# Optimization experiments

Hardware: AMD Instinct MI355X
Metric: run time of the kernel (lower is better)

The kernel has to match this reference:

```python
import jax, jax.numpy as jnp
import numpy as np

EPS_ATTN = 1e-6
EPS_LN = 1e-5


def _layer_norm(x, g, b):
    m = jnp.mean(x, axis=-1, keepdims=True)
    v = jnp.mean((x - m) ** 2, axis=-1, keepdims=True)
    return (x - m) * jax.lax.rsqrt(v + EPS_LN) * g + b


def _linear_attention(q, k, v):
    # q,k,v: [N, L/S, H, D]; elu feature map (+1 keeps values positive)
    q = jax.nn.elu(q) + 1.0
    k = jax.nn.elu(k) + 1.0
    s_len = v.shape[1]
    v = v / s_len
    kv = jnp.einsum('nshd,nshv->nhdv', k, v)            # [N,H,D,D]
    z = 1.0 / (jnp.einsum('nlhd,nhd->nlh', q, k.sum(axis=1)) + EPS_ATTN)
    out = jnp.einsum('nlhd,nhdv->nlhv', q, kv) * z[..., None] * s_len
    return out


def setup_inputs() -> dict:
    key = jax.random.key(0)
    ks = jax.random.split(key, 8)
    N, L, S, H, D = 4, 4096, 4096, 8, 64
    sc = 0.05
    return {
        'x': jax.random.normal(ks[0], (N, L, H, D), jnp.float32),
        'source': jax.random.normal(ks[1], (N, S, H, D), jnp.float32),
        'wq': jax.random.normal(ks[2], (D, D), jnp.float32) * sc,
        'wk': jax.random.normal(ks[3], (D, D), jnp.float32) * sc,
        'wv': jax.random.normal(ks[4], (D, D), jnp.float32) * sc,
        'wmerge': jax.random.normal(ks[5], (D, D), jnp.float32) * sc,
        'w1': jax.random.normal(ks[6], (2 * D, 2 * D), jnp.float32) * sc,
        'w2': jax.random.normal(ks[7], (D, 2 * D), jnp.float32) * sc,
        'g1': jnp.ones((D,), jnp.float32),
        'b1': jnp.zeros((D,), jnp.float32),
        'g2': jnp.ones((D,), jnp.float32),
        'b2': jnp.zeros((D,), jnp.float32),
    }


def reference(x, source, wq, wk, wv, wmerge, w1, w2, g1, b1, g2, b2):
    # projections (torch Linear: y = x @ W.T), applied on last dim D=d_model
    q = jnp.einsum('nlhd,ed->nlhe', x, wq)
    k = jnp.einsum('nshd,ed->nshe', source, wk)
    v = jnp.einsum('nshd,ed->nshe', source, wv)
    message = _linear_attention(q, k, v)                # [N,L,H,D]
    message = jnp.einsum('nlhd,ed->nlhe', message, wmerge)
    message = _layer_norm(message, g1, b1)
    h = jnp.concatenate([x, message], axis=-1)          # [N,L,H,2D]
    h = jax.nn.relu(jnp.einsum('nlhd,ed->nlhe', h, w1))
    h = jnp.einsum('nlhd,ed->nlhe', h, w2)              # [N,L,H,D]
    h = _layer_norm(h, g2, b2)
    return x + h
```

## Files before the change

### kernel.cpp

```cpp
#include <hip/hip_runtime.h>
#include <cstdint>

#define NB 4
#define LL 4096
#define SS 4096
#define HH 8
#define DD 64
#define NHC (NB*HH)

typedef unsigned short ushort_t;
typedef __bf16 bf16x8 __attribute__((ext_vector_type(8)));
typedef float f32x4 __attribute__((ext_vector_type(4)));
typedef unsigned short u16x8 __attribute__((ext_vector_type(8)));

__device__ __forceinline__ float bf2f(unsigned short u) {
    union { unsigned int i; float f; } v; v.i = ((unsigned int)u) << 16; return v.f;
}
__device__ __forceinline__ unsigned short f2bf(float f) {
    union { float ff; unsigned int i; } v; v.ff = f;
    unsigned int x = v.i;
    x += 0x7fffu + ((x >> 16) & 1u);
    return (unsigned short)(x >> 16);
}
__device__ __forceinline__ bool input_is_bf16(const void* g1) {
    return ((const unsigned short*)g1)[0] == 0x3F80u;
}

template<bool BF16>
__device__ __forceinline__ float ldgf(const void* p, size_t i) {
    if constexpr (BF16) return bf2f(((const unsigned short*)p)[i]);
    else                return ((const float*)p)[i];
}
template<bool BF16>
__device__ __forceinline__ u16x8 ld8(const void* p, size_t i) {
    if constexpr (BF16) {
        return *reinterpret_cast<const u16x8*>((const unsigned short*)p + i);
    } else {
        const float* f = (const float*)p + i;
        u16x8 o;
        #pragma unroll
        for (int j = 0; j < 8; ++j) o[j] = f2bf(f[j]);
        return o;
    }
}
__device__ __forceinline__ bf16x8 ldsA(const ushort_t* p) {
    return *reinterpret_cast<const bf16x8*>(p);
}
#define MFMA16(a,b,c) __builtin_amdgcn_mfma_f32_16x16x32_bf16(a,b,c,0,0,0)

template<bool BF16, int LC>
__device__ __forceinline__ void stage_w(const void* g, size_t goff, ushort_t* dst,
                                        int rows, int dstride, int tid) {
    int total8 = (rows << LC) >> 3;
    for (int i8 = tid; i8 < total8; i8 += 256) {
        int i = i8 << 3;
        int r = i >> LC, c = i & ((1 << LC) - 1);
        *reinterpret_cast<u16x8*>(dst + r * dstride + c) = ld8<BF16>(g, goff + i);
    }
}

__device__ __forceinline__ void red16(float v[4]) {
    #pragma unroll
    for (int m = 1; m < 16; m <<= 1) {
        #pragma unroll
        for (int r = 0; r < 4; ++r) v[r] += __shfl_xor(v[r], m);
    }
}

template<bool BF16>
__global__ __launch_bounds__(256, 2) void kv_kernel(
    const void* __restrict__ src, const void* __restrict__ wk, const void* __restrict__ wv,
    const void* __restrict__ g1, float* __restrict__ kvg, float* __restrict__ ksumg)
{
    if (input_is_bf16(g1) != BF16) return;
    __shared__ ushort_t S[128 * 72];
    __shared__ ushort_t KT[64 * 136];
    __shared__ ushort_t VT[64 * 136];

    const int tid = threadIdx.x;
    const int lane = tid & 63, w = tid >> 6;
    const int lg = lane >> 4, l15 = lane & 15;
    const int bid = blockIdx.x;
    const int nh = bid >> 3, ch = bid & 7;
    const int n = nh >> 3, h = nh & 7;
    const int s0 = ch * 512;
    const f32x4 z4 = {0.f, 0.f, 0.f, 0.f};

    stage_w<BF16, 6>(wk, 0, KT, 64, 136, tid);
    stage_w<BF16, 6>(wv, 0, VT, 64, 136, tid);
    __syncthreads();
    bf16x8 wkf[2][4], wvf[2][4];
    #pragma unroll
    for (int ks = 0; ks < 2; ++ks)
        #pragma unroll
        for (int nt = 0; nt < 4; ++nt) {
            wkf[ks][nt] = ldsA(KT + (nt * 16 + l15) * 136 + ks * 32 + lg * 8);
            wvf[ks][nt] = ldsA(VT + (nt * 16 + l15) * 136 + ks * 32 + lg * 8);
        }
    __syncthreads();

    float ksp[4] = {0.f, 0.f, 0.f, 0.f};
    f32x4 kvacc[4];
    #pragma unroll
    for (int nt = 0; nt < 4; ++nt) kvacc[nt] = z4;

    for (int st = 0; st < 4; ++st) {
        for (int i = tid; i < 128 * 8; i += 256) {
            int r = i >> 3, c8 = (i & 7) << 3;
            size_t gb = ((size_t)((size_t)n * SS + (s0 + st * 128 + r)) * HH + h) * DD + c8;
            *reinterpret_cast<u16x8*>(S + r * 72 + c8) = ld8<BF16>(src, gb);
        }
        __syncthreads();

        #pragma unroll
        for (int mtt = 0; mtt < 2; ++mtt) {
            const int rowA = w * 32 + mtt * 16;
            bf16x8 af[2];
            #pragma unroll
            for (int ks = 0; ks < 2; ++ks)
                af[ks] = ldsA(S + (rowA + l15) * 72 + ks * 32 + lg * 8);
            f32x4 ka[4], va[4];
            #pragma unroll
            for (int nt = 0; nt < 4; ++nt) { ka[nt] = z4; va[nt] = z4; }
            #pragma unroll
            for (int ks = 0; ks < 2; ++ks)
                #pragma unroll
                for (int nt = 0; nt < 4; ++nt) {
                    ka[nt] = MFMA16(af[ks], wkf[ks][nt], ka[nt]);
                    va[nt] = MFMA16(af[ks], wvf[ks][nt], va[nt]);
                }
            #pragma unroll
            for (int nt = 0; nt < 4; ++nt)
                #pragma unroll
                for (int r = 0; r < 4; ++r) {
                    float kvl = ka[nt][r];
                    kvl = kvl > 0.f ? kvl + 1.f : __expf(kvl);
                    ksp[nt] += kvl;
                    int srow = rowA + lg * 4 + r;
                    int dcol = nt * 16 + l15;
                    KT[dcol * 136 + srow] = f2bf(kvl);
                    VT[dcol * 136 + srow] = f2bf(va[nt][r]);
                }
        }
        __syncthreads();

        #pragma unroll
        for (int ks = 0; ks < 4; ++ks) {
            bf16x8 akv = ldsA(KT + (w * 16 + l15) * 136 + ks * 32 + lg * 8);
            #pragma unroll
            for (int nt = 0; nt < 4; ++nt) {
                bf16x8 bkv = ldsA(VT + (nt * 16 + l15) * 136 + ks * 32 + lg * 8);
                kvacc[nt] = MFMA16(akv, bkv, kvacc[nt]);
            }
        }
        __syncthreads();
    }

    float* kvo = kvg + (size_t)nh * DD * DD;
    #pragma unroll
    for (int nt = 0; nt < 4; ++nt)
        #pragma unroll
        for (int r = 0; r < 4; ++r)
            atomicAdd(&kvo[(w * 16 + lg * 4 + r) * DD + nt * 16 + l15], kvacc[nt][r]);
    #pragma unroll
    for (int m = 16; m < 64; m <<= 1)
        #pragma unroll
        for (int nt = 0; nt < 4; ++nt) ksp[nt] += __shfl_xor(ksp[nt], m);
    if (lane < 16) {
        #pragma unroll
        for (int nt = 0; nt < 4; ++nt)
            atomicAdd(&ksumg[nh * DD + nt * 16 + lane], ksp[nt]);
    }
}

template<bool BF16>
__global__ __launch_bounds__(256, 2) void main_kernel(
    const void* __restrict__ x,
    const void* __restrict__ wq, const void* __restrict__ wm,
    const void* __restrict__ w1, const void* __restrict__ w2,
    const void* __restrict__ g1, const void* __restrict__ b1,
    const void* __restrict__ g2, const void* __restrict__ b2,
    const float* __restrict__ kvg, const float* __restrict__ ksumg,
    void* __restrict__ outp)
{
    if (input_is_bf16(g1) != BF16) return;
    __shared__ ushort_t w1s[128 * 136];
    __shared__ ushort_t kvs[64 * 72];
    __shared__ ushort_t B0[64 * 72];
    __shared__ ushort_t B1[64 * 72];
    __shared__ ushort_t B2[64 * 136];

    const int tid = threadIdx.x;
    const int lane = tid & 63, w = tid >> 6;
    const int lg = lane >> 4, l15 = lane & 15;
    const int bid = blockIdx.x;
    const int nh = bid >> 4, ch = bid & 15;
    const int n = nh >> 3, h = nh & 7;
    const int rowA = w * 16;
    const f32x4 z4 = {0.f, 0.f, 0.f, 0.f};

    for (int i = tid; i < 4096; i += 256) {
        int d = i >> 6, e = i & 63;
        kvs[e * 72 + d] = f2bf(kvg[(size_t)nh * 4096 + i]);
    }
    stage_w<BF16, 7>(w1, 0, w1s, 128, 136, tid);

    bf16x8 wqf[2][4], wmf[2][4], w2f[4][4];
    stage_w<BF16, 6>(wq, 0, B0, 64, 72, tid);
    __syncthreads();
    #pragma unroll
    for (int ks = 0; ks < 2; ++ks)
        #pragma unroll
        for (int nt = 0; nt < 4; ++nt)
            wqf[ks][nt] = ldsA(B0 + (nt * 16 + l15) * 72 + ks * 32 + lg * 8);
    __syncthreads();
    stage_w<BF16, 6>(wm, 0, B0, 64, 72, tid);
    __syncthreads();
    #pragma unroll
    for (int ks = 0; ks < 2; ++ks)
        #pragma unroll
        for (int nt = 0; nt < 4; ++nt)
            wmf[ks][nt] = ldsA(B0 + (nt * 16 + l15) * 72 + ks * 32 + lg * 8);
    __syncthreads();
    stage_w<BF16, 7>(w2, 0, B2, 64, 136, tid);
    __syncthreads();
    #pragma unroll
    for (int ks = 0; ks < 4; ++ks)
        #pragma unroll
        for (int nt = 0; nt < 4; ++nt)
            w2f[ks][nt] = ldsA(B2 + (nt * 16 + l15) * 136 + ks * 32 + lg * 8);

    float g1r[4], b1r[4], g2r[4], b2r[4], ksr[4];
    #pragma unroll
    for (int nt = 0; nt < 4; ++nt) {
        int c = nt * 16 + l15;
        g1r[nt] = ldgf<BF16>(g1, c); b1r[nt] = ldgf<BF16>(b1, c);
        g2r[nt] = ldgf<BF16>(g2, c); b2r[nt] = ldgf<BF16>(b2, c);
        ksr[nt] = ksumg[nh * 64 + c];
    }
    __syncthreads();

    for (int t = 0; t < 4; ++t) {
        const int l0 = ch * 256 + t * 64;

        #pragma unroll
        for (int p = 0; p < 2; ++p) {
            int r16 = p * 8 + (lane >> 3), c8 = (lane & 7) << 3;
            size_t gb = ((size_t)((size_t)n * LL + (l0 + rowA + r16)) * HH + h) * DD + c8;
            *reinterpret_cast<u16x8*>(B0 + (rowA + r16) * 72 + c8) = ld8<BF16>(x, gb);
        }

        bf16x8 af[2];
        #pragma unroll
        for (int ks = 0; ks < 2; ++ks)
            af[ks] = ldsA(B0 + (rowA + l15) * 72 + ks * 32 + lg * 8);
        f32x4 qa[4];
        #pragma unroll
        for (int nt = 0; nt < 4; ++nt) qa[nt] = z4;
        #pragma unroll
        for (int ks = 0; ks < 2; ++ks)
            #pragma unroll
            for (int nt = 0; nt < 4; ++nt)
                qa[nt] = MFMA16(af[ks], wqf[ks][nt], qa[nt]);
        float zp[4] = {0.f, 0.f, 0.f, 0.f};
        #pragma unroll
        for (int nt = 0; nt < 4; ++nt)
            #pragma unroll
            for (int r = 0; r < 4; ++r) {
                float v = qa[nt][r];
                v = v > 0.f ? v + 1.f : __expf(v);
                qa[nt][r] = v;
                zp[r] += v * ksr[nt];
            }
        red16(zp);
        float zr[4];
        #pragma unroll
        for (int r = 0; r < 4; ++r) zr[r] = 1.f / (zp[r] + 1e-6f);
        #pragma unroll
        for (int nt = 0; nt < 4; ++nt)
            #pragma unroll
            for (int r = 0; r < 4; ++r)
                B1[(rowA + lg * 4 + r) * 72 + nt * 16 + l15] = f2bf(qa[nt][r]);

        #pragma unroll
        for (int ks = 0; ks < 2; ++ks)
            af[ks] = ldsA(B1 + (rowA + l15) * 72 + ks * 32 + lg * 8);
        f32x4 ma[4];
        #pragma unroll
        for (int nt = 0; nt < 4; ++nt) ma[nt] = z4;
        #pragma unroll
        for (int ks = 0; ks < 2; ++ks)
            #pragma unroll
            for (int nt = 0; nt < 4; ++nt) {
                bf16x8 bkv = ldsA(kvs + (nt * 16 + l15) * 72 + ks * 32 + lg * 8);
                ma[nt] = MFMA16(af[ks], bkv, ma[nt]);
            }
        #pragma unroll
        for (int nt = 0; nt < 4; ++nt)
            #pragma unroll
            for (int r = 0; r < 4; ++r)
                B1[(rowA + lg * 4 + r) * 72 + nt * 16 + l15] = f2bf(ma[nt][r] * zr[r]);

        #pragma unroll
        for (int ks = 0; ks < 2; ++ks)
            af[ks] = ldsA(B1 + (rowA + l15) * 72 + ks * 32 + lg * 8);
        f32x4 ga[4];
        #pragma unroll
        for (int nt = 0; nt < 4; ++nt) ga[nt] = z4;
        #pragma unroll
        for (int ks = 0; ks < 2; ++ks)
            #pragma unroll
            for (int nt = 0; nt < 4; ++nt)
                ga[nt] = MFMA16(af[ks], wmf[ks][nt], ga[nt]);
        float s1[4] = {0.f,0.f,0.f,0.f}, s2[4] = {0.f,0.f,0.f,0.f};
        #pragma unroll
        for (int nt = 0; nt < 4; ++nt)
            #pragma unroll
            for (int r = 0; r < 4; ++r) {
                float v = ga[nt][r]; s1[r] += v; s2[r] += v * v;
            }
        red16(s1); red16(s2);
        #pragma unroll
        for (int r = 0; r < 4; ++r) {
            float mu = s1[r] * 0.015625f;
            float var = s2[r] * 0.015625f - mu * mu;
            float rs = rsqrtf(var + 1e-5f);
            s1[r] = mu; s2[r] = rs;
        }
        #pragma unroll
        for (int nt = 0; nt < 4; ++nt)
            #pragma unroll
            for (int r = 0; r < 4; ++r)
                B1[(rowA + lg * 4 + r) * 72 + nt * 16 + l15] =
                    f2bf((ga[nt][r] - s1[r]) * s2[r] * g1r[nt] + b1r[nt]);

        #pragma unroll
        for (int half = 0; half < 2; ++half) {
            f32x4 ta[4];
            #pragma unroll
            for (int nt = 0; nt < 4; ++nt) ta[nt] = z4;
            #pragma unroll
            for (int ks = 0; ks < 4; ++ks) {
                const ushort_t* basep = (ks < 2) ? B0 : B1;
                bf16x8 a1 = ldsA(basep + (rowA + l15) * 72 + (ks & 1) * 32 + lg * 8);
                #pragma unroll
                for (int nt = 0; nt < 4; ++nt) {
                    bf16x8 bw = ldsA(w1s + (half * 64 + nt * 16 + l15) * 136 + ks * 32 + lg * 8);
                    ta[nt] = MFMA16(a1, bw, ta[nt]);
                }
            }
            #pragma unroll
            for (int nt = 0; nt < 4; ++nt)
                #pragma unroll
                for (int r = 0; r < 4; ++r)
                    B2[(rowA + lg * 4 + r) * 136 + (half * 4 + nt) * 16 + l15] =
                        f2bf(fmaxf(ta[nt][r], 0.f));
        }

        f32x4 ha[4];
        #pragma unroll
        for (int nt = 0; nt < 4; ++nt) ha[nt] = z4;
        #pragma unroll
        for (int ks = 0; ks < 4; ++ks) {
            bf16x8 a2 = ldsA(B2 + (rowA + l15) * 136 + ks * 32 + lg * 8);
            #pragma unroll
            for (int nt = 0; nt < 4; ++nt)
                ha[nt] = MFMA16(a2, w2f[ks][nt], ha[nt]);
        }
        float t1[4] = {0.f,0.f,0.f,0.f}, t2[4] = {0.f,0.f,0.f,0.f};
        #pragma unroll
        for (int nt = 0; nt < 4; ++nt)
            #pragma unroll
            for (int r = 0; r < 4; ++r) {
                float v = ha[nt][r]; t1[r] += v; t2[r] += v * v;
            }
        red16(t1); red16(t2);
        #pragma unroll
        for (int r = 0; r < 4; ++r) {
            float mu = t1[r] * 0.015625f;
            float var = t2[r] * 0.015625f - mu * mu;
            float rs = rsqrtf(var + 1e-5f);
            t1[r] = mu; t2[r] = rs;
        }
        #pragma unroll
        for (int nt = 0; nt < 4; ++nt)
            #pragma unroll
            for (int r = 0; r < 4; ++r) {
                float xv = bf2f(B0[(rowA + lg * 4 + r) * 72 + nt * 16 + l15]);
                float ov = xv + (ha[nt][r] - t1[r]) * t2[r] * g2r[nt] + b2r[nt];
                B1[(rowA + lg * 4 + r) * 72 + nt * 16 + l15] = f2bf(ov);
            }

        #pragma unroll
        for (int p = 0; p < 2; ++p) {
            int r16 = p * 8 + (lane >> 3), c8 = (lane & 7) << 3;
            size_t gb = ((size_t)((size_t)n * LL + (l0 + rowA + r16)) * HH + h) * DD + c8;
            u16x8 v = *reinterpret_cast<const u16x8*>(B1 + (rowA + r16) * 72 + c8);
            if constexpr (BF16) {
                *reinterpret_cast<u16x8*>((unsigned short*)outp + gb) = v;
            } else {
                float* fo = (float*)outp + gb;
                #pragma unroll
                for (int j = 0; j < 8; ++j) fo[j] = bf2f(v[j]);
            }
        }
    }
}

extern "C" void kernel_launch(void* const* d_in, const int* in_sizes, int n_in,
                              void* d_out, int out_size, void* d_ws, size_t ws_size,
                              hipStream_t stream) {
    const void* x   = d_in[0];
    const void* src = d_in[1];
    const void* wq  = d_in[2];
    const void* wk  = d_in[3];
    const void* wv  = d_in[4];
    const void* wm  = d_in[5];
    const void* w1  = d_in[6];
    const void* w2  = d_in[7];
    const void* g1  = d_in[8];
    const void* b1  = d_in[9];
    const void* g2  = d_in[10];
    const void* b2  = d_in[11];

    float* kvg   = (float*)d_ws;
    float* ksumg = kvg + (size_t)NHC * DD * DD;

    hipMemsetAsync(d_ws, 0, ((size_t)NHC * DD * DD + NHC * DD) * sizeof(float), stream);

    kv_kernel<true ><<<NHC * 8, 256, 0, stream>>>(src, wk, wv, g1, kvg, ksumg);
    kv_kernel<false><<<NHC * 8, 256, 0, stream>>>(src, wk, wv, g1, kvg, ksumg);
    main_kernel<true ><<<NHC * 16, 256, 0, stream>>>(x, wq, wm, w1, w2, g1, b1, g2, b2,
                                                     kvg, ksumg, d_out);
    main_kernel<false><<<NHC * 16, 256, 0, stream>>>(x, wq, wm, w1, w2, g1, b1, g2, b2,
                                                     kvg, ksumg, d_out);
}
```

Before: 170.3 us.

## Fold merge weight into KV matrix, single dtype-dispatch launches, split FFN by halves

Precomputes kv·Wmerge^T once per block so the per-tile merge projection GEMM and one LDS round-trip disappear, and the folded matrix is held in registers as MFMA B fragments. The two template launches per stage are collapsed into one kernel each that branches on input dtype at runtime, removing two empty kernel launches. The FFN second GEMM is interleaved per half so B2 shrinks to 64x72, cutting LDS use. Folding changes rounding order (kv·Wm rounded to bf16) and moves the z scaling before the merge, which is mathematically equivalent.

```diff
diff --git a/kernel.cpp b/kernel.cpp
--- a/kernel.cpp
+++ b/kernel.cpp
@@ -68,15 +68,11 @@
 }
 
 template<bool BF16>
-__global__ __launch_bounds__(256, 2) void kv_kernel(
-    const void* __restrict__ src, const void* __restrict__ wk, const void* __restrict__ wv,
-    const void* __restrict__ g1, float* __restrict__ kvg, float* __restrict__ ksumg)
+__device__ void kv_body(const void* __restrict__ src, const void* __restrict__ wk,
+                        const void* __restrict__ wv, float* __restrict__ kvg,
+                        float* __restrict__ ksumg,
+                        ushort_t* S, ushort_t* KT, ushort_t* VT)
 {
-    if (input_is_bf16(g1) != BF16) return;
-    __shared__ ushort_t S[128 * 72];
-    __shared__ ushort_t KT[64 * 136];
-    __shared__ ushort_t VT[64 * 136];
-
     const int tid = threadIdx.x;
     const int lane = tid & 63, w = tid >> 6;
     const int lg = lane >> 4, l15 = lane & 15;
@@ -99,10 +95,10 @@
         }
     __syncthreads();
 
+    f32x4 kvacc[4];
+    #pragma unroll
+    for (int nt = 0; nt < 4; ++nt) kvacc[nt] = z4;
     float ksp[4] = {0.f, 0.f, 0.f, 0.f};
-    f32x4 kvacc[4];
-    #pragma unroll
-    for (int nt = 0; nt < 4; ++nt) kvacc[nt] = z4;
 
     for (int st = 0; st < 4; ++st) {
         for (int i = tid; i < 128 * 8; i += 256) {
@@ -173,7 +169,243 @@
     }
 }
 
+__global__ __launch_bounds__(256, 2) void kv_kernel(
+    const void* __restrict__ src, const void* __restrict__ wk, const void* __restrict__ wv,
+    const void* __restrict__ g1, float* __restrict__ kvg, float* __restrict__ ksumg)
+{
+    __shared__ ushort_t S[128 * 72];
+    __shared__ ushort_t KT[64 * 136];
+    __shared__ ushort_t VT[64 * 136];
+    if (input_is_bf16(g1)) kv_body<true >(src, wk, wv, kvg, ksumg, S, KT, VT);
+    else                   kv_body<false>(src, wk, wv, kvg, ksumg, S, KT, VT);
+}
+
 template<bool BF16>
+__device__ void main_body(const void* __restrict__ x,
+                          const void* __restrict__ wq, const void* __restrict__ wm,
+                          const void* __restrict__ w1, const void* __restrict__ w2,
+                          const void* __restrict__ g1, const void* __restrict__ b1,
+                          const void* __restrict__ g2, const void* __restrict__ b2,
+                          const float* __restrict__ kvg, const float* __restrict__ ksumg,
+                          void* __restrict__ outp,
+                          ushort_t* w1s, ushort_t* kvs, ushort_t* B0, ushort_t* B1,
+                          ushort_t* B2)
+{
+    const int tid = threadIdx.x;
+    const int lane = tid & 63, w = tid >> 6;
+    const int lg = lane >> 4, l15 = lane & 15;
+    const int bid = blockIdx.x;
+    const int nh = bid >> 4, ch = bid & 15;
+    const int n = nh >> 3, h = nh & 7;
+    const int rowA = w * 16;
+    const f32x4 z4 = {0.f, 0.f, 0.f, 0.f};
+
+    stage_w<BF16, 6>(wq, 0, B0, 64, 72, tid);
+    stage_w<BF16, 6>(wm, 0, B1, 64, 72, tid);
+    stage_w<BF16, 7>(w2, 0, w1s, 64, 136, tid);
+    for (int i = tid; i < 4096; i += 256) {
+        int d = i >> 6, e = i & 63;
+        B2[d * 72 + e] = f2bf(kvg[(size_t)nh * 4096 + i]);
+    }
+    __syncthreads();
+
+    bf16x8 wqf[2][4], w2f[4][4];
+    #pragma unroll
+    for (int ks = 0; ks < 2; ++ks)
+        #pragma unroll
+        for (int nt = 0; nt < 4; ++nt)
+            wqf[ks][nt] = ldsA(B0 + (nt * 16 + l15) * 72 + ks * 32 + lg * 8);
+    #pragma unroll
+    for (int ks = 0; ks < 4; ++ks)
+        #pragma unroll
+        for (int nt = 0; nt < 4; ++nt)
+            w2f[ks][nt] = ldsA(w1s + (nt * 16 + l15) * 136 + ks * 32 + lg * 8);
+    {
+        bf16x8 akv[2];
+        #pragma unroll
+        for (int ks = 0; ks < 2; ++ks)
+            akv[ks] = ldsA(B2 + (w * 16 + l15) * 72 + ks * 32 + lg * 8);
+        f32x4 km[4];
+        #pragma unroll
+        for (int nt = 0; nt < 4; ++nt) km[nt] = z4;
+        #pragma unroll
+        for (int ks = 0; ks < 2; ++ks)
+            #pragma unroll
+            for (int nt = 0; nt < 4; ++nt) {
+                bf16x8 bwm = ldsA(B1 + (nt * 16 + l15) * 72 + ks * 32 + lg * 8);
+                km[nt] = MFMA16(akv[ks], bwm, km[nt]);
+            }
+        #pragma unroll
+        for (int nt = 0; nt < 4; ++nt)
+            #pragma unroll
+            for (int r = 0; r < 4; ++r)
+                kvs[(nt * 16 + l15) * 72 + w * 16 + lg * 4 + r] = f2bf(km[nt][r]);
+    }
+    __syncthreads();
+
+    stage_w<BF16, 7>(w1, 0, w1s, 128, 136, tid);
+    bf16x8 kvmf[2][4];
+    #pragma unroll
+    for (int ks = 0; ks < 2; ++ks)
+        #pragma unroll
+        for (int nt = 0; nt < 4; ++nt)
+            kvmf[ks][nt] = ldsA(kvs + (nt * 16 + l15) * 72 + ks * 32 + lg * 8);
+    float g1r[4], b1r[4], g2r[4], b2r[4], ksr[4];
+    #pragma unroll
+    for (int nt = 0; nt < 4; ++nt) {
+        int c = nt * 16 + l15;
+        g1r[nt] = ldgf<BF16>(g1, c); b1r[nt] = ldgf<BF16>(b1, c);
+        g2r[nt] = ldgf<BF16>(g2, c); b2r[nt] = ldgf<BF16>(b2, c);
+        ksr[nt] = ksumg[nh * 64 + c];
+    }
+    __syncthreads();
+
+    for (int t = 0; t < 4; ++t) {
+        const int l0 = ch * 256 + t * 64;
+
+        #pragma unroll
+        for (int p = 0; p < 2; ++p) {
+            int r16 = p * 8 + (lane >> 3), c8 = (lane & 7) << 3;
+            size_t gb = ((size_t)((size_t)n * LL + (l0 + rowA + r16)) * HH + h) * DD + c8;
+            *reinterpret_cast<u16x8*>(B0 + (rowA + r16) * 72 + c8) = ld8<BF16>(x, gb);
+        }
+
+        bf16x8 af[2];
+        #pragma unroll
+        for (int ks = 0; ks < 2; ++ks)
+            af[ks] = ldsA(B0 + (rowA + l15) * 72 + ks * 32 + lg * 8);
+        f32x4 qa[4];
+        #pragma unroll
+        for (int nt = 0; nt < 4; ++nt) qa[nt] = z4;
+        #pragma unroll
+        for (int ks = 0; ks < 2; ++ks)
+            #pragma unroll
+            for (int nt = 0; nt < 4; ++nt)
+                qa[nt] = MFMA16(af[ks], wqf[ks][nt], qa[nt]);
+        float zp[4] = {0.f, 0.f, 0.f, 0.f};
+        #pragma unroll
+        for (int nt = 0; nt < 4; ++nt)
+            #pragma unroll
+            for (int r = 0; r < 4; ++r) {
+                float v = qa[nt][r];
+                v = v > 0.f ? v + 1.f : __expf(v);
+                zp[r] += v * ksr[nt];
+                B1[(rowA + lg * 4 + r) * 72 + nt * 16 + l15] = f2bf(v);
+            }
+        red16(zp);
+        float zr[4];
+        #pragma unroll
+        for (int r = 0; r < 4; ++r) zr[r] = 1.f / (zp[r] + 1e-6f);
+
+        #pragma unroll
+        for (int ks = 0; ks < 2; ++ks)
+            af[ks] = ldsA(B1 + (rowA + l15) * 72 + ks * 32 + lg * 8);
+        f32x4 ma[4];
+        #pragma unroll
+        for (int nt = 0; nt < 4; ++nt) ma[nt] = z4;
+        #pragma unroll
+        for (int ks = 0; ks < 2; ++ks)
+            #pragma unroll
+            for (int nt = 0; nt < 4; ++nt)
+                ma[nt] = MFMA16(af[ks], kvmf[ks][nt], ma[nt]);
+        #pragma unroll
+        for (int nt = 0; nt < 4; ++nt)
+            #pragma unroll
+            for (int r = 0; r < 4; ++r) ma[nt][r] *= zr[r];
+
+        float s1[4] = {0.f,0.f,0.f,0.f}, s2[4] = {0.f,0.f,0.f,0.f};
+        #pragma unroll
+        for (int nt = 0; nt < 4; ++nt)
+            #pragma unroll
+            for (int r = 0; r < 4; ++r) {
+                float v = ma[nt][r]; s1[r] += v; s2[r] += v * v;
+            }
+        red16(s1); red16(s2);
+        #pragma unroll
+        for (int r = 0; r < 4; ++r) {
+            float mu = s1[r] * 0.015625f;
+            float var = s2[r] * 0.015625f - mu * mu;
+            s1[r] = mu; s2[r] = rsqrtf(var + 1e-5f);
+        }
+        #pragma unroll
+        for (int nt = 0; nt < 4; ++nt)
+            #pragma unroll
+            for (int r = 0; r < 4; ++r)
+                B1[(rowA + lg * 4 + r) * 72 + nt * 16 + l15] =
+                    f2bf((ma[nt][r] - s1[r]) * s2[r] * g1r[nt] + b1r[nt]);
+
+        f32x4 ha[4];
+        #pragma unroll
+        for (int nt = 0; nt < 4; ++nt) ha[nt] = z4;
+        #pragma unroll
+        for (int half = 0; half < 2; ++half) {
+            f32x4 ta[4];
+            #pragma unroll
+            for (int nt = 0; nt < 4; ++nt) ta[nt] = z4;
+            #pragma unroll
+            for (int ks = 0; ks < 4; ++ks) {
+                const ushort_t* bp = (ks < 2) ? B0 : B1;
+                bf16x8 a1 = ldsA(bp + (rowA + l15) * 72 + (ks & 1) * 32 + lg * 8);
+                #pragma unroll
+                for (int nt = 0; nt < 4; ++nt) {
+                    bf16x8 bw = ldsA(w1s + (half * 64 + nt * 16 + l15) * 136 + ks * 32 + lg * 8);
+                    ta[nt] = MFMA16(a1, bw, ta[nt]);
+                }
+            }
+            #pragma unroll
+            for (int nt = 0; nt < 4; ++nt)
+                #pragma unroll
+                for (int r = 0; r < 4; ++r)
+                    B2[(rowA + lg * 4 + r) * 72 + nt * 16 + l15] =
+                        f2bf(fmaxf(ta[nt][r], 0.f));
+            #pragma unroll
+            for (int k2 = 0; k2 < 2; ++k2) {
+                bf16x8 a2 = ldsA(B2 + (rowA + l15) * 72 + k2 * 32 + lg * 8);
+                #pragma unroll
+                for (int nt = 0; nt < 4; ++nt)
+                    ha[nt] = MFMA16(a2, w2f[half * 2 + k2][nt], ha[nt]);
+            }
+        }
+
+        float t1[4] = {0.f,0.f,0.f,0.f}, t2[4] = {0.f,0.f,0.f,0.f};
+        #pragma unroll
+        for (int nt = 0; nt < 4; ++nt)
+            #pragma unroll
+            for (int r = 0; r < 4; ++r) {
+                float v = ha[nt][r]; t1[r] += v; t2[r] += v * v;
+            }
+        red16(t1); red16(t2);
+        #pragma unroll
+        for (int r = 0; r < 4; ++r) {
+            float mu = t1[r] * 0.015625f;
+            float var = t2[r] * 0.015625f - mu * mu;
+            t1[r] = mu; t2[r] = rsqrtf(var + 1e-5f);
+        }
+        #pragma unroll
+        for (int nt = 0; nt < 4; ++nt)
+            #pragma unroll
+            for (int r = 0; r < 4; ++r) {
+                float xv = bf2f(B0[(rowA + lg * 4 + r) * 72 + nt * 16 + l15]);
+                float ov = xv + (ha[nt][r] - t1[r]) * t2[r] * g2r[nt] + b2r[nt];
+                B1[(rowA + lg * 4 + r) * 72 + nt * 16 + l15] = f2bf(ov);
+            }
+
+        #pragma unroll
+        for (int p = 0; p < 2; ++p) {
+            int r16 = p * 8 + (lane >> 3), c8 = (lane & 7) << 3;
+            size_t gb = ((size_t)((size_t)n * LL + (l0 + rowA + r16)) * HH + h) * DD + c8;
+            u16x8 v = *reinterpret_cast<const u16x8*>(B1 + (rowA + r16) * 72 + c8);
+            if constexpr (BF16) {
+                *reinterpret_cast<u16x8*>((unsigned short*)outp + gb) = v;
+            } else {
+                float* fo = (float*)outp + gb;
+                #pragma unroll
+                for (int j = 0; j < 8; ++j) fo[j] = bf2f(v[j]);
+            }
+        }
+    }
+}
+
 __global__ __launch_bounds__(256, 2) void main_kernel(
     const void* __restrict__ x,
     const void* __restrict__ wq, const void* __restrict__ wm,
@@ -183,228 +415,17 @@
     const float* __restrict__ kvg, const float* __restrict__ ksumg,
     void* __restrict__ outp)
 {
-    if (input_is_bf16(g1) != BF16) return;
     __shared__ ushort_t w1s[128 * 136];
     __shared__ ushort_t kvs[64 * 72];
     __shared__ ushort_t B0[64 * 72];
     __shared__ ushort_t B1[64 * 72];
-    __shared__ ushort_t B2[64 * 136];
-
-    const int tid = threadIdx.x;
-    const int lane = tid & 63, w = tid >> 6;
-    const int lg = lane >> 4, l15 = lane & 15;
-    const int bid = blockIdx.x;
-    const int nh = bid >> 4, ch = bid & 15;
-    const int n = nh >> 3, h = nh & 7;
-    const int rowA = w * 16;
-    const f32x4 z4 = {0.f, 0.f, 0.f, 0.f};
-
-    for (int i = tid; i < 4096; i += 256) {
-        int d = i >> 6, e = i & 63;
-        kvs[e * 72 + d] = f2bf(kvg[(size_t)nh * 4096 + i]);
-    }
-    stage_w<BF16, 7>(w1, 0, w1s, 128, 136, tid);
-
-    bf16x8 wqf[2][4], wmf[2][4], w2f[4][4];
-    stage_w<BF16, 6>(wq, 0, B0, 64, 72, tid);
-    __syncthreads();
-    #pragma unroll
-    for (int ks = 0; ks < 2; ++ks)
-        #pragma unroll
-        for (int nt = 0; nt < 4; ++nt)
-            wqf[ks][nt] = ldsA(B0 + (nt * 16 + l15) * 72 + ks * 32 + lg * 8);
-    __syncthreads();
-    stage_w<BF16, 6>(wm, 0, B0, 64, 72, tid);
-    __syncthreads();
-    #pragma unroll
-    for (int ks = 0; ks < 2; ++ks)
-        #pragma unroll
-        for (int nt = 0; nt < 4; ++nt)
-            wmf[ks][nt] = ldsA(B0 + (nt * 16 + l15) * 72 + ks * 32 + lg * 8);
-    __syncthreads();
-    stage_w<BF16, 7>(w2, 0, B2, 64, 136, tid);
-    __syncthreads();
-    #pragma unroll
-    for (int ks = 0; ks < 4; ++ks)
-        #pragma unroll
-        for (int nt = 0; nt < 4; ++nt)
-            w2f[ks][nt] = ldsA(B2 + (nt * 16 + l15) * 136 + ks * 32 + lg * 8);
-
-    float g1r[4], b1r[4], g2r[4], b2r[4], ksr[4];
-    #pragma unroll
-    for (int nt = 0; nt < 4; ++nt) {
-        int c = nt * 16 + l15;
-        g1r[nt] = ldgf<BF16>(g1, c); b1r[nt] = ldgf<BF16>(b1, c);
-        g2r[nt] = ldgf<BF16>(g2, c); b2r[nt] = ldgf<BF16>(b2, c);
-        ksr[nt] = ksumg[nh * 64 + c];
-    }
-    __syncthreads();
-
-    for (int t = 0; t < 4; ++t) {
-        const int l0 = ch * 256 + t * 64;
-
-        #pragma unroll
-        for (int p = 0; p < 2; ++p) {
-            int r16 = p * 8 + (lane >> 3), c8 = (lane & 7) << 3;
-            size_t gb = ((size_t)((size_t)n * LL + (l0 + rowA + r16)) * HH + h) * DD + c8;
-            *reinterpret_cast<u16x8*>(B0 + (rowA + r16) * 72 + c8) = ld8<BF16>(x, gb);
-        }
-
-        bf16x8 af[2];
-        #pragma unroll
-        for (int ks = 0; ks < 2; ++ks)
-            af[ks] = ldsA(B0 + (rowA + l15) * 72 + ks * 32 + lg * 8);
-        f32x4 qa[4];
-        #pragma unroll
-        for (int nt = 0; nt < 4; ++nt) qa[nt] = z4;
-        #pragma unroll
-        for (int ks = 0; ks < 2; ++ks)
-            #pragma unroll
-            for (int nt = 0; nt < 4; ++nt)
-                qa[nt] = MFMA16(af[ks], wqf[ks][nt], qa[nt]);
-        float zp[4] = {0.f, 0.f, 0.f, 0.f};
-        #pragma unroll
-        for (int nt = 0; nt < 4; ++nt)
-            #pragma unroll
-            for (int r = 0; r < 4; ++r) {
-                float v = qa[nt][r];
-                v = v > 0.f ? v + 1.f : __expf(v);
-                qa[nt][r] = v;
-                zp[r] += v * ksr[nt];
-            }
-        red16(zp);
-        float zr[4];
-        #pragma unroll
-        for (int r = 0; r < 4; ++r) zr[r] = 1.f / (zp[r] + 1e-6f);
-        #pragma unroll
-        for (int nt = 0; nt < 4; ++nt)
-            #pragma unroll
-            for (int r = 0; r < 4; ++r)
-                B1[(rowA + lg * 4 + r) * 72 + nt * 16 + l15] = f2bf(qa[nt][r]);
-
-        #pragma unroll
-        for (int ks = 0; ks < 2; ++ks)
-            af[ks] = ldsA(B1 + (rowA + l15) * 72 + ks * 32 + lg * 8);
-        f32x4 ma[4];
-        #pragma unroll
-        for (int nt = 0; nt < 4; ++nt) ma[nt] = z4;
-        #pragma unroll
-        for (int ks = 0; ks < 2; ++ks)
-            #pragma unroll
-            for (int nt = 0; nt < 4; ++nt) {
-                bf16x8 bkv = ldsA(kvs + (nt * 16 + l15) * 72 + ks * 32 + lg * 8);
-                ma[nt] = MFMA16(af[ks], bkv, ma[nt]);
-            }
-        #pragma unroll
-        for (int nt = 0; nt < 4; ++nt)
-            #pragma unroll
-            for (int r = 0; r < 4; ++r)
-                B1[(rowA + lg * 4 + r) * 72 + nt * 16 + l15] = f2bf(ma[nt][r] * zr[r]);
-
-        #pragma unroll
-        for (int ks = 0; ks < 2; ++ks)
-            af[ks] = ldsA(B1 + (rowA + l15) * 72 + ks * 32 + lg * 8);
-        f32x4 ga[4];
-        #pragma unroll
-        for (int nt = 0; nt < 4; ++nt) ga[nt] = z4;
-        #pragma unroll
-        for (int ks = 0; ks < 2; ++ks)
-            #pragma unroll
-            for (int nt = 0; nt < 4; ++nt)
-                ga[nt] = MFMA16(af[ks], wmf[ks][nt], ga[nt]);
-        float s1[4] = {0.f,0.f,0.f,0.f}, s2[4] = {0.f,0.f,0.f,0.f};
-        #pragma unroll
-        for (int nt = 0; nt < 4; ++nt)
-            #pragma unroll
-            for (int r = 0; r < 4; ++r) {
-                float v = ga[nt][r]; s1[r] += v; s2[r] += v * v;
-            }
-        red16(s1); red16(s2);
-        #pragma unroll
-        for (int r = 0; r < 4; ++r) {
-            float mu = s1[r] * 0.015625f;
-            float var = s2[r] * 0.015625f - mu * mu;
-            float rs = rsqrtf(var + 1e-5f);
-            s1[r] = mu; s2[r] = rs;
-        }
-        #pragma unroll
-        for (int nt = 0; nt < 4; ++nt)
-            #pragma unroll
-            for (int r = 0; r < 4; ++r)
-                B1[(rowA + lg * 4 + r) * 72 + nt * 16 + l15] =
-                    f2bf((ga[nt][r] - s1[r]) * s2[r] * g1r[nt] + b1r[nt]);
-
-        #pragma unroll
-        for (int half = 0; half < 2; ++half) {
-            f32x4 ta[4];
-            #pragma unroll
-            for (int nt = 0; nt < 4; ++nt) ta[nt] = z4;
-            #pragma unroll
-            for (int ks = 0; ks < 4; ++ks) {
-                const ushort_t* basep = (ks < 2) ? B0 : B1;
-                bf16x8 a1 = ldsA(basep + (rowA + l15) * 72 + (ks & 1) * 32 + lg * 8);
-                #pragma unroll
-                for (int nt = 0; nt < 4; ++nt) {
-                    bf16x8 bw = ldsA(w1s + (half * 64 + nt * 16 + l15) * 136 + ks * 32 + lg * 8);
-                    ta[nt] = MFMA16(a1, bw, ta[nt]);
-                }
-            }
-            #pragma unroll
-            for (int nt = 0; nt < 4; ++nt)
-                #pragma unroll
-                for (int r = 0; r < 4; ++r)
-                    B2[(rowA + lg * 4 + r) * 136 + (half * 4 + nt) * 16 + l15] =
-                        f2bf(fmaxf(ta[nt][r], 0.f));
-        }
-
-        f32x4 ha[4];
-        #pragma unroll
-        for (int nt = 0; nt < 4; ++nt) ha[nt] = z4;
-        #pragma unroll
-        for (int ks = 0; ks < 4; ++ks) {
-            bf16x8 a2 = ldsA(B2 + (rowA + l15) * 136 + ks * 32 + lg * 8);
-            #pragma unroll
-            for (int nt = 0; nt < 4; ++nt)
-                ha[nt] = MFMA16(a2, w2f[ks][nt], ha[nt]);
-        }
-        float t1[4] = {0.f,0.f,0.f,0.f}, t2[4] = {0.f,0.f,0.f,0.f};
-        #pragma unroll
-        for (int nt = 0; nt < 4; ++nt)
-            #pragma unroll
-            for (int r = 0; r < 4; ++r) {
-                float v = ha[nt][r]; t1[r] += v; t2[r] += v * v;
-            }
-        red16(t1); red16(t2);
-        #pragma unroll
-        for (int r = 0; r < 4; ++r) {
-            float mu = t1[r] * 0.015625f;
-            float var = t2[r] * 0.015625f - mu * mu;
-            float rs = rsqrtf(var + 1e-5f);
-            t1[r] = mu; t2[r] = rs;
-        }
-        #pragma unroll
-        for (int nt = 0; nt < 4; ++nt)
-            #pragma unroll
-            for (int r = 0; r < 4; ++r) {
-                float xv = bf2f(B0[(rowA + lg * 4 + r) * 72 + nt * 16 + l15]);
-                float ov = xv + (ha[nt][r] - t1[r]) * t2[r] * g2r[nt] + b2r[nt];
-                B1[(rowA + lg * 4 + r) * 72 + nt * 16 + l15] = f2bf(ov);
-            }
-
-        #pragma unroll
-        for (int p = 0; p < 2; ++p) {
-            int r16 = p * 8 + (lane >> 3), c8 = (lane & 7) << 3;
-            size_t gb = ((size_t)((size_t)n * LL + (l0 + rowA + r16)) * HH + h) * DD + c8;
-            u16x8 v = *reinterpret_cast<const u16x8*>(B1 + (rowA + r16) * 72 + c8);
-            if constexpr (BF16) {
-                *reinterpret_cast<u16x8*>((unsigned short*)outp + gb) = v;
-            } else {
-                float* fo = (float*)outp + gb;
-                #pragma unroll
-                for (int j = 0; j < 8; ++j) fo[j] = bf2f(v[j]);
-            }
-        }
-    }
+    __shared__ ushort_t B2[64 * 72];
+    if (input_is_bf16(g1))
+        main_body<true >(x, wq, wm, w1, w2, g1, b1, g2, b2, kvg, ksumg, outp,
+                         w1s, kvs, B0, B1, B2);
+    else
+        main_body<false>(x, wq, wm, w1, w2, g1, b1, g2, b2, kvg, ksumg, outp,
+                         w1s, kvs, B0, B1, B2);
 }
 
 extern "C" void kernel_launch(void* const* d_in, const int* in_sizes, int n_in,
@@ -427,11 +448,7 @@
     float* ksumg = kvg + (size_t)NHC * DD * DD;
 
     hipMemsetAsync(d_ws, 0, ((size_t)NHC * DD * DD + NHC * DD) * sizeof(float), stream);
-
-    kv_kernel<true ><<<NHC * 8, 256, 0, stream>>>(src, wk, wv, g1, kvg, ksumg);
-    kv_kernel<false><<<NHC * 8, 256, 0, stream>>>(src, wk, wv, g1, kvg, ksumg);
-    main_kernel<true ><<<NHC * 16, 256, 0, stream>>>(x, wq, wm, w1, w2, g1, b1, g2, b2,
-                                                     kvg, ksumg, d_out);
-    main_kernel<false><<<NHC * 16, 256, 0, stream>>>(x, wq, wm, w1, w2, g1, b1, g2, b2,
-                                                     kvg, ksumg, d_out);
-}
+    kv_kernel<<<NHC * 8, 256, 0, stream>>>(src, wk, wv, g1, kvg, ksumg);
+    main_kernel<<<NHC * 16, 256, 0, stream>>>(x, wq, wm, w1, w2, g1, b1, g2, b2,
+                                              kvg, ksumg, d_out);
+}
```

After: 165.0 us. 1.03x faster.
